# Kernel optimization log

Hardware: AMD Instinct MI355X
Metric: run time of the kernel (lower is better)

Reference implementation:

```python
import jax, jax.numpy as jnp
import numpy as np

N = 1_000_000      # total atoms
B = 1024           # number of molecules (batch segments)
NUM_ELEMENTS = 118
D_EMB = 64
D_HID = 128


def setup_inputs() -> dict:
    key = jax.random.key(0)
    ks = jax.random.split(key, 9)
    positions = jax.random.normal(ks[0], (N, 3), dtype=jnp.float32) * 5.0
    atomic_numbers = jax.random.randint(ks[1], (N,), 0, NUM_ELEMENTS, dtype=jnp.int64)
    batch = jnp.sort(jax.random.randint(ks[2], (N,), 0, B, dtype=jnp.int64))
    # learned parameters (torch Linear is y = x @ W.T + b; we store W as (in, out))
    embed = jax.random.normal(ks[3], (NUM_ELEMENTS, D_EMB), dtype=jnp.float32) * 0.1
    W1 = jax.random.normal(ks[4], (D_EMB, D_HID), dtype=jnp.float32) * (1.0 / np.sqrt(D_EMB))
    b1 = jnp.zeros((D_HID,), dtype=jnp.float32)
    W2 = jax.random.normal(ks[5], (D_HID, D_HID), dtype=jnp.float32) * (1.0 / np.sqrt(D_HID))
    b2 = jnp.zeros((D_HID,), dtype=jnp.float32)
    W3 = jax.random.normal(ks[6], (D_HID, 1), dtype=jnp.float32) * (1.0 / np.sqrt(D_HID))
    b3 = jnp.zeros((1,), dtype=jnp.float32)
    return {
        "positions": positions,
        "embed": embed,
        "W1": W1, "b1": b1,
        "W2": W2, "b2": b2,
        "W3": W3, "b3": b3,
        "atomic_numbers": atomic_numbers,
        "batch": batch,
    }


def reference(positions, embed, W1, b1, W2, b2, W3, b3, atomic_numbers, batch):
    def energy_fn(pos):
        h = embed[atomic_numbers]                       # [N, 64] gather
        pos_feat = jnp.sum(pos, axis=-1, keepdims=True) # [N, 1]
        h = h + 0.0 * pos_feat                          # keeps pos in the graph (grad is zero)
        x = jax.nn.silu(h @ W1 + b1)                    # [N, 128]
        x = jax.nn.silu(x @ W2 + b2)                    # [N, 128]
        per_atom = (x @ W3 + b3)[:, 0]                  # [N]
        # energy.scatter_add_(0, batch, per_atom)
        return jax.ops.segment_sum(per_atom, batch, num_segments=B)  # [B]

    energy = energy_fn(positions)
    # forces = -grad_R sum(V(R)); identically zero here but computed faithfully
    forces = -jax.grad(lambda p: energy_fn(p).sum())(positions)      # [N, 3]
    return (energy, forces)
```

## Files before the change

### kernel.cpp

```cpp
#include <hip/hip_runtime.h>

#define D_EMB   64
#define D_HID   128
#define NUM_EL  118
#define PREP_GRID 2048

__global__ __launch_bounds__(256)
void mace_prep_kernel(const float* __restrict__ embed,
                      const float* __restrict__ W1, const float* __restrict__ b1,
                      const float* __restrict__ W2, const float* __restrict__ b2,
                      const float* __restrict__ W3, const float* __restrict__ b3,
                      float* __restrict__ Etab,
                      float4* __restrict__ forces4, int nf4) {
    const int t = threadIdx.x;

    const int gstride = gridDim.x * blockDim.x;
    for (int i = blockIdx.x * blockDim.x + t; i < nf4; i += gstride)
        forces4[i] = make_float4(0.f, 0.f, 0.f, 0.f);

    if (blockIdx.x < NUM_EL) {
        __shared__ float h[D_EMB];
        __shared__ float x1[D_HID];
        __shared__ float wsum[2];
        const int z = blockIdx.x;

        if (t < D_EMB) h[t] = embed[z * D_EMB + t];
        __syncthreads();

        if (t < D_HID) {
            float a0 = 0.f, a1 = 0.f, a2 = 0.f, a3 = 0.f;
            #pragma unroll
            for (int k = 0; k < D_EMB; k += 4) {
                a0 = fmaf(h[k + 0], W1[(k + 0) * D_HID + t], a0);
                a1 = fmaf(h[k + 1], W1[(k + 1) * D_HID + t], a1);
                a2 = fmaf(h[k + 2], W1[(k + 2) * D_HID + t], a2);
                a3 = fmaf(h[k + 3], W1[(k + 3) * D_HID + t], a3);
            }
            const float acc = b1[t] + ((a0 + a1) + (a2 + a3));
            x1[t] = acc / (1.0f + expf(-acc));
        }
        __syncthreads();

        float r = 0.f;
        if (t < D_HID) {
            float a0 = 0.f, a1 = 0.f, a2 = 0.f, a3 = 0.f;
            #pragma unroll
            for (int k = 0; k < D_HID; k += 4) {
                a0 = fmaf(x1[k + 0], W2[(k + 0) * D_HID + t], a0);
                a1 = fmaf(x1[k + 1], W2[(k + 1) * D_HID + t], a1);
                a2 = fmaf(x1[k + 2], W2[(k + 2) * D_HID + t], a2);
                a3 = fmaf(x1[k + 3], W2[(k + 3) * D_HID + t], a3);
            }
            const float acc2 = b2[t] + ((a0 + a1) + (a2 + a3));
            const float s2 = acc2 / (1.0f + expf(-acc2));
            r = s2 * W3[t];
        }
        #pragma unroll
        for (int off = 32; off > 0; off >>= 1)
            r += __shfl_down(r, off, 64);
        if (t < D_HID && (t & 63) == 0) wsum[t >> 6] = r;
        __syncthreads();
        if (t == 0) Etab[z] = wsum[0] + wsum[1] + b3[0];
    }
}

__device__ __forceinline__ int lower_bound_wave(const int* __restrict__ arr,
                                                int n, int target) {
    int lo = 0, hi = n;
    const int lane = threadIdx.x & 63;
    while (hi > lo) {
        const int range = hi - lo;
        const int step  = (range + 63) >> 6;
        const int pos   = lo + lane * step;
        const bool lt   = (pos < hi) && (arr[pos] < target);
        const unsigned long long m = __ballot(lt);
        const int k = __popcll(m);
        if (k == 0) { hi = lo; break; }
        const int new_lo = lo + (k - 1) * step + 1;
        int new_hi = lo + k * step;
        if (new_hi > hi) new_hi = hi;
        lo = new_lo; hi = new_hi;
    }
    return lo;
}

__global__ __launch_bounds__(256)
void mace_segsum_kernel(const int* __restrict__ z,
                        const int* __restrict__ batch,
                        const float* __restrict__ EtabG,
                        float* __restrict__ energy, int n) {
    __shared__ float etab_s[NUM_EL];
    __shared__ int   bounds[2];
    __shared__ float wsum[4];
    const int b = blockIdx.x;
    const int t = threadIdx.x;
    const int w = t >> 6;

    if (t < NUM_EL) etab_s[t] = EtabG[t];

    if (w == 0) {
        const int s = lower_bound_wave(batch, n, b);
        if ((t & 63) == 0) bounds[0] = s;
    } else if (w == 1) {
        const int e = lower_bound_wave(batch, n, b + 1);
        if ((t & 63) == 0) bounds[1] = e;
    }
    __syncthreads();

    const int start = bounds[0], end = bounds[1];
    float acc = 0.f;

    int a0 = (start + 3) & ~3;
    if (a0 > end) a0 = end;
    const int a1 = (end >= a0) ? (end & ~3) : a0;

    if (t < a0 - start) acc += etab_s[z[start + t]];
    if (a1 >= a0 && t < end - a1) acc += etab_s[z[a1 + t]];
    const int4* __restrict__ z4 = (const int4*)z;
    for (int i4 = (a0 >> 2) + t; i4 < (a1 >> 2); i4 += 256) {
        const int4 v = z4[i4];
        acc += etab_s[v.x] + etab_s[v.y] + etab_s[v.z] + etab_s[v.w];
    }

    #pragma unroll
    for (int off = 32; off > 0; off >>= 1)
        acc += __shfl_down(acc, off, 64);
    if ((t & 63) == 0) wsum[w] = acc;
    __syncthreads();
    if (t == 0) energy[b] = wsum[0] + wsum[1] + wsum[2] + wsum[3];
}

extern "C" void kernel_launch(void* const* d_in, const int* in_sizes, int n_in,
                              void* d_out, int out_size, void* d_ws, size_t ws_size,
                              hipStream_t stream) {
    const float* embed = (const float*)d_in[1];
    const float* W1    = (const float*)d_in[2];
    const float* b1    = (const float*)d_in[3];
    const float* W2    = (const float*)d_in[4];
    const float* b2    = (const float*)d_in[5];
    const float* W3    = (const float*)d_in[6];
    const float* b3    = (const float*)d_in[7];
    const int*   z     = (const int*)d_in[8];
    const int*   batch = (const int*)d_in[9];
    const int    n     = in_sizes[8];

    const int B   = out_size - 3 * n;
    const int nf4 = (3 * n) / 4;

    float*  energy  = (float*)d_out;
    float4* forces4 = (float4*)((float*)d_out + B);
    float*  Etab    = (float*)d_ws;

    mace_prep_kernel<<<PREP_GRID, 256, 0, stream>>>(embed, W1, b1, W2, b2, W3, b3,
                                                    Etab, forces4, nf4);
    mace_segsum_kernel<<<B, 256, 0, stream>>>(z, batch, Etab, energy, n);
}
```

Measured before the change: 14.64 us.

## Compute segment boundaries in prep kernel instead of per-block binary search

```diff
diff --git a/kernel.cpp b/kernel.cpp
--- a/kernel.cpp
+++ b/kernel.cpp
@@ -11,20 +11,36 @@
                       const float* __restrict__ W2, const float* __restrict__ b2,
                       const float* __restrict__ W3, const float* __restrict__ b3,
                       float* __restrict__ Etab,
+                      int* __restrict__ starts,
+                      const int* __restrict__ batch, int n, int B,
                       float4* __restrict__ forces4, int nf4) {
     const int t = threadIdx.x;
+    const int gid = blockIdx.x * blockDim.x + t;
+    const int gstride = gridDim.x * blockDim.x;
 
-    const int gstride = gridDim.x * blockDim.x;
-    for (int i = blockIdx.x * blockDim.x + t; i < nf4; i += gstride)
+    for (int i = gid; i < nf4; i += gstride)
         forces4[i] = make_float4(0.f, 0.f, 0.f, 0.f);
+
+    for (int i = gid; i < n - 1; i += gstride) {
+        const int c0 = batch[i];
+        const int c1 = batch[i + 1];
+        if (c0 != c1) {
+            for (int b = c0 + 1; b <= c1; ++b) starts[b] = i + 1;
+        }
+    }
+    if (gid == 0) {
+        const int first = batch[0], last = batch[n - 1];
+        for (int b = 0; b <= first; ++b) starts[b] = 0;
+        for (int b = last + 1; b <= B; ++b) starts[b] = n;
+    }
 
     if (blockIdx.x < NUM_EL) {
         __shared__ float h[D_EMB];
         __shared__ float x1[D_HID];
         __shared__ float wsum[2];
-        const int z = blockIdx.x;
+        const int zz = blockIdx.x;
 
-        if (t < D_EMB) h[t] = embed[z * D_EMB + t];
+        if (t < D_EMB) h[t] = embed[zz * D_EMB + t];
         __syncthreads();
 
         if (t < D_HID) {
@@ -60,54 +76,26 @@
             r += __shfl_down(r, off, 64);
         if (t < D_HID && (t & 63) == 0) wsum[t >> 6] = r;
         __syncthreads();
-        if (t == 0) Etab[z] = wsum[0] + wsum[1] + b3[0];
+        if (t == 0) Etab[zz] = wsum[0] + wsum[1] + b3[0];
     }
-}
-
-__device__ __forceinline__ int lower_bound_wave(const int* __restrict__ arr,
-                                                int n, int target) {
-    int lo = 0, hi = n;
-    const int lane = threadIdx.x & 63;
-    while (hi > lo) {
-        const int range = hi - lo;
-        const int step  = (range + 63) >> 6;
-        const int pos   = lo + lane * step;
-        const bool lt   = (pos < hi) && (arr[pos] < target);
-        const unsigned long long m = __ballot(lt);
-        const int k = __popcll(m);
-        if (k == 0) { hi = lo; break; }
-        const int new_lo = lo + (k - 1) * step + 1;
-        int new_hi = lo + k * step;
-        if (new_hi > hi) new_hi = hi;
-        lo = new_lo; hi = new_hi;
-    }
-    return lo;
 }
 
 __global__ __launch_bounds__(256)
 void mace_segsum_kernel(const int* __restrict__ z,
-                        const int* __restrict__ batch,
+                        const int* __restrict__ starts,
                         const float* __restrict__ EtabG,
-                        float* __restrict__ energy, int n) {
+                        float* __restrict__ energy) {
     __shared__ float etab_s[NUM_EL];
-    __shared__ int   bounds[2];
     __shared__ float wsum[4];
     const int b = blockIdx.x;
     const int t = threadIdx.x;
     const int w = t >> 6;
 
     if (t < NUM_EL) etab_s[t] = EtabG[t];
-
-    if (w == 0) {
-        const int s = lower_bound_wave(batch, n, b);
-        if ((t & 63) == 0) bounds[0] = s;
-    } else if (w == 1) {
-        const int e = lower_bound_wave(batch, n, b + 1);
-        if ((t & 63) == 0) bounds[1] = e;
-    }
+    const int start = starts[b];
+    const int end   = starts[b + 1];
     __syncthreads();
 
-    const int start = bounds[0], end = bounds[1];
     float acc = 0.f;
 
     int a0 = (start + 3) & ~3;
@@ -116,10 +104,11 @@
 
     if (t < a0 - start) acc += etab_s[z[start + t]];
     if (a1 >= a0 && t < end - a1) acc += etab_s[z[a1 + t]];
+
     const int4* __restrict__ z4 = (const int4*)z;
     for (int i4 = (a0 >> 2) + t; i4 < (a1 >> 2); i4 += 256) {
         const int4 v = z4[i4];
-        acc += etab_s[v.x] + etab_s[v.y] + etab_s[v.z] + etab_s[v.w];
+        acc += (etab_s[v.x] + etab_s[v.y]) + (etab_s[v.z] + etab_s[v.w]);
     }
 
     #pragma unroll
@@ -127,7 +116,7 @@
         acc += __shfl_down(acc, off, 64);
     if ((t & 63) == 0) wsum[w] = acc;
     __syncthreads();
-    if (t == 0) energy[b] = wsum[0] + wsum[1] + wsum[2] + wsum[3];
+    if (t == 0) energy[b] = (wsum[0] + wsum[1]) + (wsum[2] + wsum[3]);
 }
 
 extern "C" void kernel_launch(void* const* d_in, const int* in_sizes, int n_in,
@@ -150,8 +139,10 @@
     float*  energy  = (float*)d_out;
     float4* forces4 = (float4*)((float*)d_out + B);
     float*  Etab    = (float*)d_ws;
+    int*    starts  = (int*)d_ws + 128;
 
     mace_prep_kernel<<<PREP_GRID, 256, 0, stream>>>(embed, W1, b1, W2, b2, W3, b3,
-                                                    Etab, forces4, nf4);
-    mace_segsum_kernel<<<B, 256, 0, stream>>>(z, batch, Etab, energy, n);
+                                                    Etab, starts, batch, n, B,
+                                                    forces4, nf4);
+    mace_segsum_kernel<<<B, 256, 0, stream>>>(z, starts, Etab, energy);
 }
```

Result: faster. 14.10 us (-3.7%).
